# Kernel tuning notes

Hardware: AMD Instinct MI355X
Metric: run time of the kernel (lower is better)

Reference implementation:

```python
import jax, jax.numpy as jnp
import numpy as np

N_C, N_M, N_D = 100000, 50000, 10000
E = 800000
F_IN, F_H, F_OUT = 128, 64, 64
EPS = 1e-12


def setup_inputs() -> dict:
    key = jax.random.key(0)
    ks = jax.random.split(key, 24)
    s = 1.0 / np.sqrt(F_IN)
    s2 = 1.0 / np.sqrt(F_H)
    inp = {
        'x_circ': jax.random.normal(ks[0], (N_C, F_IN), jnp.float32),
        'x_mir': jax.random.normal(ks[1], (N_M, F_IN), jnp.float32),
        'x_dis': jax.random.normal(ks[2], (N_D, F_IN), jnp.float32),
        'src_cm': jax.random.randint(ks[3], (E,), 0, N_C, jnp.int32),
        'dst_cm': jax.random.randint(ks[4], (E,), 0, N_M, jnp.int32),
        'src_md': jax.random.randint(ks[5], (E,), 0, N_M, jnp.int32),
        'dst_md': jax.random.randint(ks[6], (E,), 0, N_D, jnp.int32),
        'src_cd': jax.random.randint(ks[7], (E,), 0, N_C, jnp.int32),
        'dst_cd': jax.random.randint(ks[8], (E,), 0, N_D, jnp.int32),
        'src_mc': jax.random.randint(ks[9], (E,), 0, N_M, jnp.int32),
        'dst_mc': jax.random.randint(ks[10], (E,), 0, N_C, jnp.int32),
        'src_dm': jax.random.randint(ks[11], (E,), 0, N_D, jnp.int32),
        'dst_dm': jax.random.randint(ks[12], (E,), 0, N_M, jnp.int32),
        'src_dc': jax.random.randint(ks[13], (E,), 0, N_D, jnp.int32),
        'dst_dc': jax.random.randint(ks[14], (E,), 0, N_C, jnp.int32),
        'W1_l': jax.random.uniform(ks[15], (6, F_IN, F_H), jnp.float32, -s, s),
        'W1_r': jax.random.uniform(ks[16], (6, F_IN, F_H), jnp.float32, -s, s),
        'b1': jnp.zeros((6, F_H), jnp.float32),
        'W2_l': jax.random.uniform(ks[17], (6, F_H, F_OUT), jnp.float32, -s2, s2),
        'W2_r': jax.random.uniform(ks[18], (6, F_H, F_OUT), jnp.float32, -s2, s2),
        'b2': jnp.zeros((6, F_OUT), jnp.float32),
        'W_res': jax.random.uniform(ks[19], (3, F_IN, F_OUT), jnp.float32, -s, s),
        'b_res': jnp.zeros((3, F_OUT), jnp.float32),
    }
    return inp


def _sage(x_src, x_dst, src, dst, Wl, bl, Wr, n_dst):
    # PyG SAGEConv (mean aggr): lin_l(mean_{j in N(i)} x_j) + lin_r(x_i)
    msg = x_src[src]                                              # [E, F] gather
    agg = jax.ops.segment_sum(msg, dst, num_segments=n_dst)      # [n_dst, F]
    cnt = jax.ops.segment_sum(jnp.ones_like(dst, dtype=x_src.dtype), dst,
                              num_segments=n_dst)
    mean = agg / jnp.maximum(cnt, 1.0)[:, None]
    return mean @ Wl + bl + x_dst @ Wr


def _hetero_layer(xc, xm, xd, Wl, Wr, b, edges):
    # relation order: 0=c->m, 1=m->d, 2=c->d, 3=m->c, 4=d->m, 5=d->c
    h_m = 0.5 * (_sage(xc, xm, edges['cm'][0], edges['cm'][1], Wl[0], b[0], Wr[0], xm.shape[0])
                 + _sage(xd, xm, edges['dm'][0], edges['dm'][1], Wl[4], b[4], Wr[4], xm.shape[0]))
    h_d = 0.5 * (_sage(xm, xd, edges['md'][0], edges['md'][1], Wl[1], b[1], Wr[1], xd.shape[0])
                 + _sage(xc, xd, edges['cd'][0], edges['cd'][1], Wl[2], b[2], Wr[2], xd.shape[0]))
    h_c = 0.5 * (_sage(xm, xc, edges['mc'][0], edges['mc'][1], Wl[3], b[3], Wr[3], xc.shape[0])
                 + _sage(xd, xc, edges['dc'][0], edges['dc'][1], Wl[5], b[5], Wr[5], xc.shape[0]))
    return h_c, h_m, h_d


def _l2norm(x):
    n = jnp.sqrt(jnp.sum(x * x, axis=1, keepdims=True))
    return x / jnp.maximum(n, EPS)


def reference(x_circ, x_mir, x_dis,
              src_cm, dst_cm, src_md, dst_md, src_cd, dst_cd,
              src_mc, dst_mc, src_dm, dst_dm, src_dc, dst_dc,
              W1_l, W1_r, b1, W2_l, W2_r, b2, W_res, b_res):
    edges = {'cm': (src_cm, dst_cm), 'md': (src_md, dst_md), 'cd': (src_cd, dst_cd),
             'mc': (src_mc, dst_mc), 'dm': (src_dm, dst_dm), 'dc': (src_dc, dst_dc)}
    h_c, h_m, h_d = _hetero_layer(x_circ, x_mir, x_dis, W1_l, W1_r, b1, edges)
    h_c, h_m, h_d = jax.nn.relu(h_c), jax.nn.relu(h_m), jax.nn.relu(h_d)  # dropout = identity (eval)
    o_c, o_m, o_d = _hetero_layer(h_c, h_m, h_d, W2_l, W2_r, b2, edges)
    o_c = o_c + x_circ @ W_res[0] + b_res[0]
    o_m = o_m + x_mir @ W_res[1] + b_res[1]
    o_d = o_d + x_dis @ W_res[2] + b_res[2]
    return _l2norm(o_c), _l2norm(o_m), _l2norm(o_d)
```

## Files before the change

### kernel.cpp

```cpp
#include <hip/hip_runtime.h>
#include <cstdint>
#include <cstddef>

#define EE        800000
#define NC        100000
#define NM        50000
#define ND        10000
#define NSLOTS    320000

#define SB0 0
#define SB1 50000
#define SB2 60000
#define SB3 70000
#define SB4 170000
#define SB5 220000

#define R0 0
#define R1 100000
#define R2 150000
#define R3 250000
#define R4 300000
#define R5 310000

#define NB 2400
#define EPB 4096
#define EBL 196
#define EPB2 8192
#define PBL 98
#define BCAP 3072

typedef _Float16 f16x8 __attribute__((ext_vector_type(8)));
typedef float f32x4 __attribute__((ext_vector_type(4)));
typedef float f32x2 __attribute__((ext_vector_type(2)));

__device__ __forceinline__ void bucket_split(int rel, int d, int& lb, int& dl) {
    switch (rel) {
        case 0: case 4: lb = d / 125; dl = d - lb * 125; break;
        case 1: case 2: lb = d / 25;  dl = d - lb * 25;  break;
        default:        lb = d / 250; dl = d - lb * 250; break;
    }
}

__global__ __launch_bounds__(256) void bucket_hist_k(
    const int* __restrict__ d0, const int* __restrict__ d1, const int* __restrict__ d2,
    const int* __restrict__ d3, const int* __restrict__ d4, const int* __restrict__ d5,
    int* __restrict__ bhist)
{
    __shared__ int hl[400];
    int rel = blockIdx.y;
    const int* dst;
    switch (rel) {
        case 0: dst = d0; break; case 1: dst = d1; break; case 2: dst = d2; break;
        case 3: dst = d3; break; case 4: dst = d4; break; default: dst = d5; break;
    }
    int tid = threadIdx.x;
    for (int i = tid; i < 400; i += 256) hl[i] = 0;
    __syncthreads();
    int e0 = blockIdx.x * EPB;
#pragma unroll
    for (int t = 0; t < EPB / 256; ++t) {
        int e = e0 + t * 256 + tid;
        if (e < EE) {
            int lb, dl;
            bucket_split(rel, dst[e], lb, dl);
            atomicAdd(&hl[lb], 1);
        }
    }
    __syncthreads();
    for (int i = tid; i < 400; i += 256) {
        int v = hl[i];
        if (v) atomicAdd(&bhist[rel * 400 + i], v);
    }
}

__global__ __launch_bounds__(256) void bucket_scan_k(const int* __restrict__ bhist,
    int* __restrict__ bOff, int* __restrict__ bCur, int* __restrict__ off)
{
    __shared__ int lds[256];
    int tid = threadIdx.x;
    int v[10];
    int tot = 0;
#pragma unroll
    for (int t = 0; t < 10; ++t) {
        int idx = tid * 10 + t;
        int x = (idx < NB) ? bhist[idx] : 0;
        v[t] = tot;
        tot += x;
    }
    lds[tid] = tot;
    __syncthreads();
    for (int o = 1; o < 256; o <<= 1) {
        int x = 0;
        if (tid >= o) x = lds[tid - o];
        __syncthreads();
        lds[tid] += x;
        __syncthreads();
    }
    int excl = lds[tid] - tot;
#pragma unroll
    for (int t = 0; t < 10; ++t) {
        int idx = tid * 10 + t;
        if (idx < NB) {
            int val = excl + v[t];
            bOff[idx] = val;
            bCur[idx] = val;
        }
    }
    if (tid == 255) {
        bOff[NB] = lds[255];
        off[NSLOTS] = lds[255];
    }
}

__global__ __launch_bounds__(512) void partition_k(
    const int* __restrict__ s0, const int* __restrict__ d0,
    const int* __restrict__ s1, const int* __restrict__ d1,
    const int* __restrict__ s2, const int* __restrict__ d2,
    const int* __restrict__ s3, const int* __restrict__ d3,
    const int* __restrict__ s4, const int* __restrict__ d4,
    const int* __restrict__ s5, const int* __restrict__ d5,
    int* __restrict__ bCur, int* __restrict__ bArr)
{
    __shared__ int hist[400];
    __shared__ int curs[400];
    __shared__ unsigned short lbs[EPB2];
    __shared__ unsigned char dls[EPB2];
    int rel = blockIdx.y;
    const int* src; const int* dst;
    switch (rel) {
        case 0: src = s0; dst = d0; break;
        case 1: src = s1; dst = d1; break;
        case 2: src = s2; dst = d2; break;
        case 3: src = s3; dst = d3; break;
        case 4: src = s4; dst = d4; break;
        default: src = s5; dst = d5; break;
    }
    int tid = threadIdx.x;
    for (int i = tid; i < 400; i += 512) hist[i] = 0;
    __syncthreads();
    int e0 = blockIdx.x * EPB2;
    int e1 = e0 + EPB2; if (e1 > EE) e1 = EE;
    int m = e1 - e0;
    for (int i = tid; i < m; i += 512) {
        int lb, dl;
        bucket_split(rel, dst[e0 + i], lb, dl);
        lbs[i] = (unsigned short)lb;
        dls[i] = (unsigned char)dl;
        atomicAdd(&hist[lb], 1);
    }
    __syncthreads();
    for (int i = tid; i < 400; i += 512) {
        int c = hist[i];
        curs[i] = c ? atomicAdd(&bCur[rel * 400 + i], c) : 0;
    }
    __syncthreads();
    for (int i = tid; i < m; i += 512) {
        int p = atomicAdd(&curs[lbs[i]], 1);
        bArr[p] = ((int)dls[i] << 17) | src[e0 + i];
    }
}

__global__ __launch_bounds__(256) void bucket_build_k(
    const int* __restrict__ bArr, const int* __restrict__ bOff,
    int* __restrict__ off, int* __restrict__ csr)
{
    __shared__ int cnt[256];
    __shared__ int sc[256];
    __shared__ int cur[256];
    __shared__ int stage[BCAP];
    int b = blockIdx.x;
    int tid = threadIdx.x;
    int r = b / 400;
    int lb = b - r * 400;
    int spb, sbase;
    switch (r) {
        case 0: spb = 125; sbase = SB0; break;
        case 1: spb = 25;  sbase = SB1; break;
        case 2: spb = 25;  sbase = SB2; break;
        case 3: spb = 250; sbase = SB3; break;
        case 4: spb = 125; sbase = SB4; break;
        default: spb = 250; sbase = SB5; break;
    }
    int slot0 = lb * spb;
    int e0 = bOff[b], e1 = bOff[b + 1];
    int m = e1 - e0;
    int ms = m < BCAP ? m : BCAP;

    cnt[tid] = 0;
    __syncthreads();
    for (int i = tid; i < ms; i += 256) {
        int p = bArr[e0 + i];
        stage[i] = p;
        atomicAdd(&cnt[p >> 17], 1);
    }
    for (int i = BCAP + tid; i < m; i += 256) {
        int p = bArr[e0 + i];
        atomicAdd(&cnt[p >> 17], 1);
    }
    __syncthreads();
    int x = cnt[tid];
    sc[tid] = x;
    __syncthreads();
    for (int o = 1; o < 256; o <<= 1) {
        int y = 0;
        if (tid >= o) y = sc[tid - o];
        __syncthreads();
        sc[tid] += y;
        __syncthreads();
    }
    int excl = sc[tid] - x;
    cur[tid] = excl;
    if (tid < spb) off[sbase + slot0 + tid] = e0 + excl;
    __syncthreads();
    for (int i = tid; i < ms; i += 256) {
        int p = stage[i];
        int pos = atomicAdd(&cur[p >> 17], 1);
        csr[e0 + pos] = (p & 0x1FFFF) << 7;
    }
    for (int i = BCAP + tid; i < m; i += 256) {
        int p = bArr[e0 + i];
        int pos = atomicAdd(&cur[p >> 17], 1);
        csr[e0 + pos] = (p & 0x1FFFF) << 7;
    }
}

__device__ __forceinline__ unsigned f2bf(float f) {
    unsigned b = __float_as_uint(f);
    return (b + 0x7FFFu + ((b >> 16) & 1u)) >> 16;
}

__global__ __launch_bounds__(256) void cvtW_k(
    const float* __restrict__ W1l, const float* __restrict__ W2l,
    const float* __restrict__ W1r, const float* __restrict__ W2r,
    const float* __restrict__ Wres, const float* __restrict__ b1,
    const float* __restrict__ b2, const float* __restrict__ bres,
    _Float16* __restrict__ Wt1, _Float16* __restrict__ Wt2,
    _Float16* __restrict__ Wz1t, _Float16* __restrict__ Wz2t,
    _Float16* __restrict__ Wrest, float* __restrict__ bz1, float* __restrict__ bz2,
    int* __restrict__ bhist)
{
    const int raT[3] = {0, 1, 3}, rbT[3] = {4, 2, 5}, rmT[3] = {1, 2, 0};
    int i = blockIdx.x * 256 + threadIdx.x;
    if (i < NB) bhist[i] = 0;
    if (i < 6 * 128 * 64) {
        int r = i >> 13, rem = i & 8191, k = rem >> 6, n = rem & 63;
        Wt1[(size_t)r * 8192 + (size_t)n * 128 + k] = (_Float16)W1l[i];
    }
    if (i < 6 * 64 * 64) {
        int r = i >> 12, rem = i & 4095, k = rem >> 6, n = rem & 63;
        Wt2[(size_t)r * 4096 + (size_t)n * 64 + k] = (_Float16)W2l[i];
    }
    if (i < 3 * 8192) {
        int t = i >> 13, rem = i & 8191, n = rem >> 7, k = rem & 127;
        float v = 0.5f * (W1r[(size_t)raT[t] * 8192 + k * 64 + n] +
                          W1r[(size_t)rbT[t] * 8192 + k * 64 + n]);
        Wz1t[i] = (_Float16)v;
    }
    if (i < 3 * 4096) {
        int t = i >> 12, rem = i & 4095, n = rem >> 6, k = rem & 63;
        float v = 0.5f * (W2r[(size_t)raT[t] * 4096 + k * 64 + n] +
                          W2r[(size_t)rbT[t] * 4096 + k * 64 + n]);
        Wz2t[i] = (_Float16)v;
    }
    if (i < 3 * 8192) {
        int t = i >> 13, rem = i & 8191, n = rem >> 7, k = rem & 127;
        Wrest[i] = (_Float16)Wres[(size_t)rmT[t] * 8192 + k * 64 + n];
    }
    if (i < 192) {
        int t = i >> 6, n = i & 63;
        bz1[i] = 0.5f * (b1[raT[t] * 64 + n] + b1[rbT[t] * 64 + n]);
        bz2[i] = 0.5f * (b2[raT[t] * 64 + n] + b2[rbT[t] * 64 + n]) + bres[rmT[t] * 64 + n];
    }
}

__global__ __launch_bounds__(256) void fused1_k(
    const float* __restrict__ fc, const float* __restrict__ fm, const float* __restrict__ fd,
    const _Float16* __restrict__ Wt1, const _Float16* __restrict__ Wz1t,
    const float* __restrict__ bz1,
    unsigned short* __restrict__ y,
    float* __restrict__ hc, float* __restrict__ hm, float* __restrict__ hd)
{
    int b = blockIdx.x;
    int t, lb;
    if (b < 782)      { t = 0; lb = b; }
    else if (b < 939) { t = 1; lb = b - 782; }
    else              { t = 2; lb = b - 939; }
    const float* x; int n; float* zo; int ra, rb, roA, roB;
    switch (t) {
        case 0: x = fm; n = NM; zo = hm; ra = 1; rb = 3; roA = R1; roB = R3; break;
        case 1: x = fd; n = ND; zo = hd; ra = 4; rb = 5; roA = R4; roB = R5; break;
        default: x = fc; n = NC; zo = hc; ra = 0; rb = 2; roA = R0; roB = R2; break;
    }
    __shared__ _Float16 xs[64 * 136];
    int tid = threadIdx.x;
    int node0 = lb * 64;
    for (int idx = tid; idx < 64 * 16; idx += 256) {
        int nn = idx >> 4, c8 = idx & 15;
        int g = node0 + nn;
        float4 u0 = make_float4(0.f, 0.f, 0.f, 0.f), u1 = u0;
        if (g < n) {
            const float4* p = (const float4*)(x + (size_t)g * 128 + c8 * 8);
            u0 = p[0]; u1 = p[1];
        }
        f16x8 v;
        v[0] = (_Float16)u0.x; v[1] = (_Float16)u0.y; v[2] = (_Float16)u0.z; v[3] = (_Float16)u0.w;
        v[4] = (_Float16)u1.x; v[5] = (_Float16)u1.y; v[6] = (_Float16)u1.z; v[7] = (_Float16)u1.w;
        *(f16x8*)(xs + nn * 136 + c8 * 8) = v;
    }
    __syncthreads();
    int lane = tid & 63, wv = tid >> 6;
    int lr = lane & 15, lg = lane >> 4;
    if (wv < 2) {
        int rel = wv ? rb : ra;
        int ro  = wv ? roB : roA;
        const _Float16* W = Wt1 + (size_t)rel * 8192;
        unsigned short* yo = y + (size_t)ro * 64;
        f16x8 bf[4][4];
#pragma unroll
        for (int kt = 0; kt < 4; ++kt)
#pragma unroll
            for (int nt = 0; nt < 4; ++nt)
                bf[kt][nt] = *(const f16x8*)(W + (size_t)(nt * 16 + lr) * 128 + kt * 32 + lg * 8);
#pragma unroll
        for (int rt = 0; rt < 4; ++rt) {
            f32x4 acc[4];
#pragma unroll
            for (int nt = 0; nt < 4; ++nt) { acc[nt][0] = 0.f; acc[nt][1] = 0.f; acc[nt][2] = 0.f; acc[nt][3] = 0.f; }
            const _Float16* xrow = xs + (rt * 16 + lr) * 136;
#pragma unroll
            for (int kt = 0; kt < 4; ++kt) {
                f16x8 af = *(const f16x8*)(xrow + kt * 32 + lg * 8);
#pragma unroll
                for (int nt = 0; nt < 4; ++nt)
                    acc[nt] = __builtin_amdgcn_mfma_f32_16x16x32_f16(af, bf[kt][nt], acc[nt], 0, 0, 0);
            }
            int orow = node0 + rt * 16 + lg * 4;
#pragma unroll
            for (int rg = 0; rg < 4; ++rg) {
                int gg = orow + rg;
                if (gg < n) {
                    unsigned short* yr = yo + (size_t)gg * 64 + lr;
#pragma unroll
                    for (int nt = 0; nt < 4; ++nt)
                        yr[nt * 16] = (unsigned short)f2bf(acc[nt][rg]);
                }
            }
        }
    } else {
        const _Float16* W = Wz1t + (size_t)t * 8192;
        const float* bz = bz1 + t * 64;
        f16x8 bf[4][4];
#pragma unroll
        for (int kt = 0; kt < 4; ++kt)
#pragma unroll
            for (int nt = 0; nt < 4; ++nt)
                bf[kt][nt] = *(const f16x8*)(W + (size_t)(nt * 16 + lr) * 128 + kt * 32 + lg * 8);
        int rbase = (wv - 2) * 32;
#pragma unroll
        for (int rt = 0; rt < 2; ++rt) {
            f32x4 acc[4];
#pragma unroll
            for (int nt = 0; nt < 4; ++nt) {
                float bv = bz[nt * 16 + lr];
                acc[nt][0] = bv; acc[nt][1] = bv; acc[nt][2] = bv; acc[nt][3] = bv;
            }
            const _Float16* xrow = xs + (rbase + rt * 16 + lr) * 136;
#pragma unroll
            for (int kt = 0; kt < 4; ++kt) {
                f16x8 af = *(const f16x8*)(xrow + kt * 32 + lg * 8);
#pragma unroll
                for (int nt = 0; nt < 4; ++nt)
                    acc[nt] = __builtin_amdgcn_mfma_f32_16x16x32_f16(af, bf[kt][nt], acc[nt], 0, 0, 0);
            }
            int orow = node0 + rbase + rt * 16 + lg * 4;
#pragma unroll
            for (int rg = 0; rg < 4; ++rg) {
                int gg = orow + rg;
                if (gg < n) {
                    float* zr = zo + (size_t)gg * 64 + lr;
#pragma unroll
                    for (int nt = 0; nt < 4; ++nt)
                        zr[nt * 16] = acc[nt][rg];
                }
            }
        }
    }
}

__global__ __launch_bounds__(256) void fused2_k(
    const float* __restrict__ hc, const float* __restrict__ hm, const float* __restrict__ hd,
    const float* __restrict__ xc, const float* __restrict__ xm, const float* __restrict__ xd,
    const _Float16* __restrict__ Wt2, const _Float16* __restrict__ Wz2t,
    const _Float16* __restrict__ Wrest, const float* __restrict__ bz2,
    unsigned short* __restrict__ y,
    float* __restrict__ oc, float* __restrict__ om, float* __restrict__ od)
{
    int b = blockIdx.x;
    int t, lb;
    if (b < 782)      { t = 0; lb = b; }
    else if (b < 939) { t = 1; lb = b - 782; }
    else              { t = 2; lb = b - 939; }
    const float *h, *x; int n; float* zo; int ra, rb, roA, roB;
    switch (t) {
        case 0: h = hm; x = xm; n = NM; zo = om; ra = 1; rb = 3; roA = R1; roB = R3; break;
        case 1: h = hd; x = xd; n = ND; zo = od; ra = 4; rb = 5; roA = R4; roB = R5; break;
        default: h = hc; x = xc; n = NC; zo = oc; ra = 0; rb = 2; roA = R0; roB = R2; break;
    }
    __shared__ _Float16 hs[64 * 72];
    __shared__ _Float16 xs[64 * 136];
    int tid = threadIdx.x;
    int node0 = lb * 64;
    for (int idx = tid; idx < 64 * 8; idx += 256) {
        int nn = idx >> 3, c8 = idx & 7;
        int g = node0 + nn;
        float4 u0 = make_float4(0.f, 0.f, 0.f, 0.f), u1 = u0;
        if (g < n) {
            const float4* p = (const float4*)(h + (size_t)g * 64 + c8 * 8);
            u0 = p[0]; u1 = p[1];
        }
        f16x8 v;
        v[0] = (_Float16)u0.x; v[1] = (_Float16)u0.y; v[2] = (_Float16)u0.z; v[3] = (_Float16)u0.w;
        v[4] = (_Float16)u1.x; v[5] = (_Float16)u1.y; v[6] = (_Float16)u1.z; v[7] = (_Float16)u1.w;
        *(f16x8*)(hs + nn * 72 + c8 * 8) = v;
    }
    for (int idx = tid; idx < 64 * 16; idx += 256) {
        int nn = idx >> 4, c8 = idx & 15;
        int g = node0 + nn;
        float4 u0 = make_float4(0.f, 0.f, 0.f, 0.f), u1 = u0;
        if (g < n) {
            const float4* p = (const float4*)(x + (size_t)g * 128 + c8 * 8);
            u0 = p[0]; u1 = p[1];
        }
        f16x8 v;
        v[0] = (_Float16)u0.x; v[1] = (_Float16)u0.y; v[2] = (_Float16)u0.z; v[3] = (_Float16)u0.w;
        v[4] = (_Float16)u1.x; v[5] = (_Float16)u1.y; v[6] = (_Float16)u1.z; v[7] = (_Float16)u1.w;
        *(f16x8*)(xs + nn * 136 + c8 * 8) = v;
    }
    __syncthreads();
    int lane = tid & 63, wv = tid >> 6;
    int lr = lane & 15, lg = lane >> 4;
    if (wv < 2) {
        int rel = wv ? rb : ra;
        int ro  = wv ? roB : roA;
        const _Float16* W = Wt2 + (size_t)rel * 4096;
        unsigned short* yo = y + (size_t)ro * 64;
        f16x8 bf[2][4];
#pragma unroll
        for (int kt = 0; kt < 2; ++kt)
#pragma unroll
            for (int nt = 0; nt < 4; ++nt)
                bf[kt][nt] = *(const f16x8*)(W + (size_t)(nt * 16 + lr) * 64 + kt * 32 + lg * 8);
#pragma unroll
        for (int rt = 0; rt < 4; ++rt) {
            f32x4 acc[4];
#pragma unroll
            for (int nt = 0; nt < 4; ++nt) { acc[nt][0] = 0.f; acc[nt][1] = 0.f; acc[nt][2] = 0.f; acc[nt][3] = 0.f; }
            const _Float16* hrow = hs + (rt * 16 + lr) * 72;
#pragma unroll
            for (int kt = 0; kt < 2; ++kt) {
                f16x8 af = *(const f16x8*)(hrow + kt * 32 + lg * 8);
#pragma unroll
                for (int nt = 0; nt < 4; ++nt)
                    acc[nt] = __builtin_amdgcn_mfma_f32_16x16x32_f16(af, bf[kt][nt], acc[nt], 0, 0, 0);
            }
            int orow = node0 + rt * 16 + lg * 4;
#pragma unroll
            for (int rg = 0; rg < 4; ++rg) {
                int gg = orow + rg;
                if (gg < n) {
                    unsigned short* yr = yo + (size_t)gg * 64 + lr;
#pragma unroll
                    for (int nt = 0; nt < 4; ++nt)
                        yr[nt * 16] = (unsigned short)f2bf(acc[nt][rg]);
                }
            }
        }
    } else {
        const _Float16* Wh = Wz2t + (size_t)t * 4096;
        const _Float16* Wx = Wrest + (size_t)t * 8192;
        const float* bz = bz2 + t * 64;
        f16x8 bfh[2][4];
#pragma unroll
        for (int kt = 0; kt < 2; ++kt)
#pragma unroll
            for (int nt = 0; nt < 4; ++nt)
                bfh[kt][nt] = *(const f16x8*)(Wh + (size_t)(nt * 16 + lr) * 64 + kt * 32 + lg * 8);
        f16x8 bfx[4][4];
#pragma unroll
        for (int kt = 0; kt < 4; ++kt)
#pragma unroll
            for (int nt = 0; nt < 4; ++nt)
                bfx[kt][nt] = *(const f16x8*)(Wx + (size_t)(nt * 16 + lr) * 128 + kt * 32 + lg * 8);
        int rbase = (wv - 2) * 32;
#pragma unroll
        for (int rt = 0; rt < 2; ++rt) {
            f32x4 acc[4];
#pragma unroll
            for (int nt = 0; nt < 4; ++nt) {
                float bv = bz[nt * 16 + lr];
                acc[nt][0] = bv; acc[nt][1] = bv; acc[nt][2] = bv; acc[nt][3] = bv;
            }
            const _Float16* hrow = hs + (rbase + rt * 16 + lr) * 72;
            const _Float16* xrow = xs + (rbase + rt * 16 + lr) * 136;
#pragma unroll
            for (int kt = 0; kt < 2; ++kt) {
                f16x8 af = *(const f16x8*)(hrow + kt * 32 + lg * 8);
#pragma unroll
                for (int nt = 0; nt < 4; ++nt)
                    acc[nt] = __builtin_amdgcn_mfma_f32_16x16x32_f16(af, bfh[kt][nt], acc[nt], 0, 0, 0);
            }
#pragma unroll
            for (int kt = 0; kt < 4; ++kt) {
                f16x8 af = *(const f16x8*)(xrow + kt * 32 + lg * 8);
#pragma unroll
                for (int nt = 0; nt < 4; ++nt)
                    acc[nt] = __builtin_amdgcn_mfma_f32_16x16x32_f16(af, bfx[kt][nt], acc[nt], 0, 0, 0);
            }
            int orow = node0 + rbase + rt * 16 + lg * 4;
#pragma unroll
            for (int rg = 0; rg < 4; ++rg) {
                int gg = orow + rg;
                if (gg < n) {
                    float* zr = zo + (size_t)gg * 64 + lr;
#pragma unroll
                    for (int nt = 0; nt < 4; ++nt)
                        zr[nt * 16] = acc[nt][rg];
                }
            }
        }
    }
}

__device__ __forceinline__ void acc_pk(f32x2* a, uint4 v) {
    f32x2 t0, t1, t2, t3;
    t0[0] = __uint_as_float(v.x << 16); t0[1] = __uint_as_float(v.x & 0xFFFF0000u);
    t1[0] = __uint_as_float(v.y << 16); t1[1] = __uint_as_float(v.y & 0xFFFF0000u);
    t2[0] = __uint_as_float(v.z << 16); t2[1] = __uint_as_float(v.z & 0xFFFF0000u);
    t3[0] = __uint_as_float(v.w << 16); t3[1] = __uint_as_float(v.w & 0xFFFF0000u);
    a[0] += t0; a[1] += t1; a[2] += t2; a[3] += t3;
}

template<bool RELU, bool NORM>
__global__ __launch_bounds__(256) void agg_all_k(
    const unsigned short* __restrict__ y, const int* __restrict__ off,
    const int* __restrict__ csr,
    float* __restrict__ ioc, float* __restrict__ iom, float* __restrict__ iod)
{
    int w = blockIdx.x * 4 + (threadIdx.x >> 6);
    int t, wid;
    if (w < NM) { t = 0; wid = w; }
    else if (w < NM + ND) { t = 1; wid = w - NM; }
    else { t = 2; wid = w - NM - ND; }
    const int *o1, *o2; const unsigned short *y1, *y2; float* io;
    switch (t) {
        case 0: o1 = off + SB0; o2 = off + SB4; y1 = y + (size_t)R0 * 64; y2 = y + (size_t)R4 * 64; io = iom; break;
        case 1: o1 = off + SB1; o2 = off + SB2; y1 = y + (size_t)R1 * 64; y2 = y + (size_t)R2 * 64; io = iod; break;
        default: o1 = off + SB3; o2 = off + SB5; y1 = y + (size_t)R3 * 64; y2 = y + (size_t)R5 * 64; io = ioc; break;
    }
    int lane = threadIdx.x & 63;
    int g = lane >> 3, ql = lane & 7;
    int qoff = ql * 16;
    f32x2 acc[4];
#pragma unroll
    for (int j = 0; j < 4; ++j) { acc[j][0] = 0.f; acc[j][1] = 0.f; }
    {
        const char* yb = (const char*)y1;
        int e0 = o1[wid], e1 = o1[wid + 1];
        f32x2 a[4];
#pragma unroll
        for (int j = 0; j < 4; ++j) { a[j][0] = 0.f; a[j][1] = 0.f; }
        int e = e0 + g;
        int i0 = 0, i1 = 0;
        if (e < e1) i0 = csr[e];
        if (e + 8 < e1) i1 = csr[e + 8];
        for (; e + 8 < e1; e += 16) {
            int p0 = csr[e + 16 < e1 ? e + 16 : e];
            int p1 = csr[e + 24 < e1 ? e + 24 : e];
            uint4 vA = *(const uint4*)(yb + (unsigned)i0 + qoff);
            uint4 vB = *(const uint4*)(yb + (unsigned)i1 + qoff);
            acc_pk(a, vA);
            acc_pk(a, vB);
            i0 = p0; i1 = p1;
        }
        if (e < e1) {
            uint4 v = *(const uint4*)(yb + (unsigned)i0 + qoff);
            acc_pk(a, v);
        }
        float inv = 1.f / fmaxf((float)(e1 - e0), 1.f);
        f32x2 iv; iv[0] = inv; iv[1] = inv;
#pragma unroll
        for (int j = 0; j < 4; ++j) acc[j] += a[j] * iv;
    }
    {
        const char* yb = (const char*)y2;
        int e0 = o2[wid], e1 = o2[wid + 1];
        f32x2 a[4];
#pragma unroll
        for (int j = 0; j < 4; ++j) { a[j][0] = 0.f; a[j][1] = 0.f; }
        int e = e0 + g;
        int i0 = 0, i1 = 0;
        if (e < e1) i0 = csr[e];
        if (e + 8 < e1) i1 = csr[e + 8];
        for (; e + 8 < e1; e += 16) {
            int p0 = csr[e + 16 < e1 ? e + 16 : e];
            int p1 = csr[e + 24 < e1 ? e + 24 : e];
            uint4 vA = *(const uint4*)(yb + (unsigned)i0 + qoff);
            uint4 vB = *(const uint4*)(yb + (unsigned)i1 + qoff);
            acc_pk(a, vA);
            acc_pk(a, vB);
            i0 = p0; i1 = p1;
        }
        if (e < e1) {
            uint4 v = *(const uint4*)(yb + (unsigned)i0 + qoff);
            acc_pk(a, v);
        }
        float inv = 1.f / fmaxf((float)(e1 - e0), 1.f);
        f32x2 iv; iv[0] = inv; iv[1] = inv;
#pragma unroll
        for (int j = 0; j < 4; ++j) acc[j] += a[j] * iv;
    }
#pragma unroll
    for (int j = 0; j < 4; ++j) {
#pragma unroll
        for (int c = 0; c < 2; ++c) {
            float v = acc[j][c];
            v += __shfl_xor(v, 8);
            v += __shfl_xor(v, 16);
            v += __shfl_xor(v, 32);
            acc[j][c] = v;
        }
    }
    if (g == 0) {
        float* iorow = io + ((size_t)wid << 6) + ql * 8;
        float4 z1 = *((const float4*)iorow);
        float4 z2 = *((const float4*)(iorow + 4));
        float o[8];
        o[0] = 0.5f * acc[0][0] + z1.x; o[1] = 0.5f * acc[0][1] + z1.y;
        o[2] = 0.5f * acc[1][0] + z1.z; o[3] = 0.5f * acc[1][1] + z1.w;
        o[4] = 0.5f * acc[2][0] + z2.x; o[5] = 0.5f * acc[2][1] + z2.y;
        o[6] = 0.5f * acc[3][0] + z2.z; o[7] = 0.5f * acc[3][1] + z2.w;
        if (RELU) {
#pragma unroll
            for (int j = 0; j < 8; ++j) o[j] = fmaxf(o[j], 0.f);
        }
        if (NORM) {
            float ss = 0.f;
#pragma unroll
            for (int j = 0; j < 8; ++j) ss += o[j] * o[j];
            ss += __shfl_xor(ss, 1); ss += __shfl_xor(ss, 2); ss += __shfl_xor(ss, 4);
            float r = 1.f / fmaxf(sqrtf(ss), 1e-12f);
#pragma unroll
            for (int j = 0; j < 8; ++j) o[j] *= r;
        }
        *((float4*)iorow) = make_float4(o[0], o[1], o[2], o[3]);
        *((float4*)(iorow + 4)) = make_float4(o[4], o[5], o[6], o[7]);
    }
}

extern "C" void kernel_launch(void* const* d_in, const int* in_sizes, int n_in,
                              void* d_out, int out_size, void* d_ws, size_t ws_size,
                              hipStream_t stream) {
    const float* x_c = (const float*)d_in[0];
    const float* x_m = (const float*)d_in[1];
    const float* x_d = (const float*)d_in[2];
    const int* src_cm = (const int*)d_in[3];
    const int* dst_cm = (const int*)d_in[4];
    const int* src_md = (const int*)d_in[5];
    const int* dst_md = (const int*)d_in[6];
    const int* src_cd = (const int*)d_in[7];
    const int* dst_cd = (const int*)d_in[8];
    const int* src_mc = (const int*)d_in[9];
    const int* dst_mc = (const int*)d_in[10];
    const int* src_dm = (const int*)d_in[11];
    const int* dst_dm = (const int*)d_in[12];
    const int* src_dc = (const int*)d_in[13];
    const int* dst_dc = (const int*)d_in[14];
    const float* W1l = (const float*)d_in[15];
    const float* W1r = (const float*)d_in[16];
    const float* b1 = (const float*)d_in[17];
    const float* W2l = (const float*)d_in[18];
    const float* W2r = (const float*)d_in[19];
    const float* b2 = (const float*)d_in[20];
    const float* Wres = (const float*)d_in[21];
    const float* bres = (const float*)d_in[22];
    float* out = (float*)d_out;

    int* off = (int*)d_ws;
    int* csr = off + 320064;
    int* bhist = csr + 4800000;
    int* bOff = bhist + 2400;
    int* bCur = bOff + 2404;
    float* h = (float*)(bCur + 2404);
    float* h_c = h;
    float* h_m = h_c + (size_t)NC * 64;
    float* h_d = h_m + (size_t)NM * 64;
    unsigned short* y = (unsigned short*)(h + (size_t)160000 * 64);
    int* bArr = (int*)y;
    _Float16* Wt1 = (_Float16*)(y + (size_t)320000 * 64);
    _Float16* Wt2 = Wt1 + 6 * 64 * 128;
    _Float16* Wz1t = Wt2 + 6 * 64 * 64;
    _Float16* Wz2t = Wz1t + 3 * 64 * 128;
    _Float16* Wrest = Wz2t + 3 * 64 * 64;
    float* bz1 = (float*)(Wrest + 3 * 64 * 128);
    float* bz2 = bz1 + 192;

    float* out_c = out;
    float* out_m = out + (size_t)NC * 64;
    float* out_d = out_m + (size_t)NM * 64;

    cvtW_k<<<192, 256, 0, stream>>>(W1l, W2l, W1r, W2r, Wres, b1, b2, bres,
                                    Wt1, Wt2, Wz1t, Wz2t, Wrest, bz1, bz2, bhist);

    bucket_hist_k<<<dim3(EBL, 6), 256, 0, stream>>>(dst_cm, dst_md, dst_cd, dst_mc, dst_dm, dst_dc, bhist);
    bucket_scan_k<<<1, 256, 0, stream>>>(bhist, bOff, bCur, off);
    partition_k<<<dim3(PBL, 6), 512, 0, stream>>>(src_cm, dst_cm, src_md, dst_md, src_cd, dst_cd,
                                                  src_mc, dst_mc, src_dm, dst_dm, src_dc, dst_dc,
                                                  bCur, bArr);
    bucket_build_k<<<NB, 256, 0, stream>>>(bArr, bOff, off, csr);

    fused1_k<<<2502, 256, 0, stream>>>(x_c, x_m, x_d, Wt1, Wz1t, bz1, y, h_c, h_m, h_d);
    agg_all_k<true, false><<<40000, 256, 0, stream>>>(y, off, csr, h_c, h_m, h_d);

    fused2_k<<<2502, 256, 0, stream>>>(h_c, h_m, h_d, x_c, x_m, x_d,
                                       Wt2, Wz2t, Wrest, bz2, y, out_c, out_m, out_d);
    agg_all_k<false, true><<<40000, 256, 0, stream>>>(y, off, csr, out_c, out_m, out_d);
}
```

Baseline: 633.8 us.

## Merge preprocessing kernels, partition concurrently with layer-1 GEMM, build CSR in place

Weight conversion is merged into the bucket histogram kernel, and edge partitioning is merged with the layer-1 projection GEMM in one launch, so independent work shares a grid and fewer kernels run. The bucket array now aliases the CSR buffer, which bucket_build_k rewrites in place after staging in LDS. BCAP is raised to 4096 and the overflow path is removed, which assumes no bucket exceeds 4096 edges. The aggregation loop drops the bounds clamps on prefetched CSR indices and folds the byte offset into the base pointer, so the last iterations may read past the end of the CSR array into the rest of the workspace.

```diff
diff --git a/kernel.cpp b/kernel.cpp
--- a/kernel.cpp
+++ b/kernel.cpp
@@ -27,7 +27,7 @@
 #define EBL 196
 #define EPB2 8192
 #define PBL 98
-#define BCAP 3072
+#define BCAP 4096
 
 typedef _Float16 f16x8 __attribute__((ext_vector_type(8)));
 typedef float f32x4 __attribute__((ext_vector_type(4)));
@@ -41,22 +41,71 @@
     }
 }
 
-__global__ __launch_bounds__(256) void bucket_hist_k(
+__device__ __forceinline__ unsigned f2bf(float f) {
+    unsigned b = __float_as_uint(f);
+    return (b + 0x7FFFu + ((b >> 16) & 1u)) >> 16;
+}
+
+__global__ __launch_bounds__(256) void cvt_hist_k(
+    const float* __restrict__ W1l, const float* __restrict__ W2l,
+    const float* __restrict__ W1r, const float* __restrict__ W2r,
+    const float* __restrict__ Wres, const float* __restrict__ b1,
+    const float* __restrict__ b2, const float* __restrict__ bres,
+    _Float16* __restrict__ Wt1, _Float16* __restrict__ Wt2,
+    _Float16* __restrict__ Wz1t, _Float16* __restrict__ Wz2t,
+    _Float16* __restrict__ Wrest, float* __restrict__ bz1, float* __restrict__ bz2,
+    int* __restrict__ bhist,
     const int* __restrict__ d0, const int* __restrict__ d1, const int* __restrict__ d2,
-    const int* __restrict__ d3, const int* __restrict__ d4, const int* __restrict__ d5,
-    int* __restrict__ bhist)
+    const int* __restrict__ d3, const int* __restrict__ d4, const int* __restrict__ d5)
 {
     __shared__ int hl[400];
-    int rel = blockIdx.y;
+    int blk = blockIdx.x;
+    int tid = threadIdx.x;
+    if (blk < 192) {
+        const int raT[3] = {0, 1, 3}, rbT[3] = {4, 2, 5}, rmT[3] = {1, 2, 0};
+        int i = blk * 256 + tid;
+        if (i < 6 * 128 * 64) {
+            int r = i >> 13, rem = i & 8191, k = rem >> 6, n = rem & 63;
+            Wt1[(size_t)r * 8192 + (size_t)n * 128 + k] = (_Float16)W1l[i];
+        }
+        if (i < 6 * 64 * 64) {
+            int r = i >> 12, rem = i & 4095, k = rem >> 6, n = rem & 63;
+            Wt2[(size_t)r * 4096 + (size_t)n * 64 + k] = (_Float16)W2l[i];
+        }
+        if (i < 3 * 8192) {
+            int t = i >> 13, rem = i & 8191, n = rem >> 7, k = rem & 127;
+            float v = 0.5f * (W1r[(size_t)raT[t] * 8192 + k * 64 + n] +
+                              W1r[(size_t)rbT[t] * 8192 + k * 64 + n]);
+            Wz1t[i] = (_Float16)v;
+        }
+        if (i < 3 * 4096) {
+            int t = i >> 12, rem = i & 4095, n = rem >> 6, k = rem & 63;
+            float v = 0.5f * (W2r[(size_t)raT[t] * 4096 + k * 64 + n] +
+                              W2r[(size_t)rbT[t] * 4096 + k * 64 + n]);
+            Wz2t[i] = (_Float16)v;
+        }
+        if (i < 3 * 8192) {
+            int t = i >> 13, rem = i & 8191, n = rem >> 7, k = rem & 127;
+            Wrest[i] = (_Float16)Wres[(size_t)rmT[t] * 8192 + k * 64 + n];
+        }
+        if (i < 192) {
+            int t = i >> 6, n = i & 63;
+            bz1[i] = 0.5f * (b1[raT[t] * 64 + n] + b1[rbT[t] * 64 + n]);
+            bz2[i] = 0.5f * (b2[raT[t] * 64 + n] + b2[rbT[t] * 64 + n]) + bres[rmT[t] * 64 + n];
+        }
+        return;
+    }
+    int hb = blk - 192;
+    int rel = hb / EBL;
+    int chunk = hb - rel * EBL;
     const int* dst;
     switch (rel) {
         case 0: dst = d0; break; case 1: dst = d1; break; case 2: dst = d2; break;
         case 3: dst = d3; break; case 4: dst = d4; break; default: dst = d5; break;
     }
-    int tid = threadIdx.x;
     for (int i = tid; i < 400; i += 256) hl[i] = 0;
     __syncthreads();
-    int e0 = blockIdx.x * EPB;
+    int e0 = chunk * EPB;
 #pragma unroll
     for (int t = 0; t < EPB / 256; ++t) {
         int e = e0 + t * 256 + tid;
@@ -112,51 +161,166 @@
     }
 }
 
-__global__ __launch_bounds__(512) void partition_k(
+__global__ __launch_bounds__(256) void part_fused1_k(
     const int* __restrict__ s0, const int* __restrict__ d0,
     const int* __restrict__ s1, const int* __restrict__ d1,
     const int* __restrict__ s2, const int* __restrict__ d2,
     const int* __restrict__ s3, const int* __restrict__ d3,
     const int* __restrict__ s4, const int* __restrict__ d4,
     const int* __restrict__ s5, const int* __restrict__ d5,
-    int* __restrict__ bCur, int* __restrict__ bArr)
+    int* __restrict__ bCur, int* __restrict__ bArr,
+    const float* __restrict__ fc, const float* __restrict__ fm, const float* __restrict__ fd,
+    const _Float16* __restrict__ Wt1, const _Float16* __restrict__ Wz1t,
+    const float* __restrict__ bz1,
+    unsigned short* __restrict__ y,
+    float* __restrict__ hc, float* __restrict__ hm, float* __restrict__ hd)
 {
-    __shared__ int hist[400];
-    __shared__ int curs[400];
-    __shared__ unsigned short lbs[EPB2];
-    __shared__ unsigned char dls[EPB2];
-    int rel = blockIdx.y;
-    const int* src; const int* dst;
-    switch (rel) {
-        case 0: src = s0; dst = d0; break;
-        case 1: src = s1; dst = d1; break;
-        case 2: src = s2; dst = d2; break;
-        case 3: src = s3; dst = d3; break;
-        case 4: src = s4; dst = d4; break;
-        default: src = s5; dst = d5; break;
-    }
+    __shared__ __align__(16) char smem[27776];
+    int blk = blockIdx.x;
     int tid = threadIdx.x;
-    for (int i = tid; i < 400; i += 512) hist[i] = 0;
-    __syncthreads();
-    int e0 = blockIdx.x * EPB2;
-    int e1 = e0 + EPB2; if (e1 > EE) e1 = EE;
-    int m = e1 - e0;
-    for (int i = tid; i < m; i += 512) {
-        int lb, dl;
-        bucket_split(rel, dst[e0 + i], lb, dl);
-        lbs[i] = (unsigned short)lb;
-        dls[i] = (unsigned char)dl;
-        atomicAdd(&hist[lb], 1);
-    }
-    __syncthreads();
-    for (int i = tid; i < 400; i += 512) {
-        int c = hist[i];
-        curs[i] = c ? atomicAdd(&bCur[rel * 400 + i], c) : 0;
-    }
-    __syncthreads();
-    for (int i = tid; i < m; i += 512) {
-        int p = atomicAdd(&curs[lbs[i]], 1);
-        bArr[p] = ((int)dls[i] << 17) | src[e0 + i];
+    if (blk < 6 * PBL) {
+        int* hist = (int*)smem;
+        int* curs = hist + 400;
+        unsigned short* lbs = (unsigned short*)(curs + 400);
+        unsigned char* dls = (unsigned char*)(lbs + EPB2);
+        int rel = blk / PBL;
+        int chunk = blk - rel * PBL;
+        const int* src; const int* dst;
+        switch (rel) {
+            case 0: src = s0; dst = d0; break;
+            case 1: src = s1; dst = d1; break;
+            case 2: src = s2; dst = d2; break;
+            case 3: src = s3; dst = d3; break;
+            case 4: src = s4; dst = d4; break;
+            default: src = s5; dst = d5; break;
+        }
+        for (int i = tid; i < 400; i += 256) hist[i] = 0;
+        __syncthreads();
+        int e0 = chunk * EPB2;
+        int e1 = e0 + EPB2; if (e1 > EE) e1 = EE;
+        int m = e1 - e0;
+        for (int i = tid; i < m; i += 256) {
+            int lb, dl;
+            bucket_split(rel, dst[e0 + i], lb, dl);
+            lbs[i] = (unsigned short)lb;
+            dls[i] = (unsigned char)dl;
+            atomicAdd(&hist[lb], 1);
+        }
+        __syncthreads();
+        for (int i = tid; i < 400; i += 256) {
+            int c = hist[i];
+            curs[i] = c ? atomicAdd(&bCur[rel * 400 + i], c) : 0;
+        }
+        __syncthreads();
+        for (int i = tid; i < m; i += 256) {
+            int p = atomicAdd(&curs[lbs[i]], 1);
+            bArr[p] = ((int)dls[i] << 17) | src[e0 + i];
+        }
+        return;
+    }
+    _Float16* xs = (_Float16*)smem;
+    int b = blk - 6 * PBL;
+    int t, lb;
+    if (b < 782)      { t = 0; lb = b; }
+    else if (b < 939) { t = 1; lb = b - 782; }
+    else              { t = 2; lb = b - 939; }
+    const float* x; int n; float* zo; int ra, rb, roA, roB;
+    switch (t) {
+        case 0: x = fm; n = NM; zo = hm; ra = 1; rb = 3; roA = R1; roB = R3; break;
+        case 1: x = fd; n = ND; zo = hd; ra = 4; rb = 5; roA = R4; roB = R5; break;
+        default: x = fc; n = NC; zo = hc; ra = 0; rb = 2; roA = R0; roB = R2; break;
+    }
+    int node0 = lb * 64;
+    for (int idx = tid; idx < 64 * 16; idx += 256) {
+        int nn = idx >> 4, c8 = idx & 15;
+        int g = node0 + nn;
+        float4 u0 = make_float4(0.f, 0.f, 0.f, 0.f), u1 = u0;
+        if (g < n) {
+            const float4* p = (const float4*)(x + (size_t)g * 128 + c8 * 8);
+            u0 = p[0]; u1 = p[1];
+        }
+        f16x8 v;
+        v[0] = (_Float16)u0.x; v[1] = (_Float16)u0.y; v[2] = (_Float16)u0.z; v[3] = (_Float16)u0.w;
+        v[4] = (_Float16)u1.x; v[5] = (_Float16)u1.y; v[6] = (_Float16)u1.z; v[7] = (_Float16)u1.w;
+        *(f16x8*)(xs + nn * 136 + c8 * 8) = v;
+    }
+    __syncthreads();
+    int lane = tid & 63, wv = tid >> 6;
+    int lr = lane & 15, lg = lane >> 4;
+    if (wv < 2) {
+        int rel = wv ? rb : ra;
+        int ro  = wv ? roB : roA;
+        const _Float16* W = Wt1 + (size_t)rel * 8192;
+        unsigned short* yo = y + (size_t)ro * 64;
+        f16x8 bf[4][4];
+#pragma unroll
+        for (int kt = 0; kt < 4; ++kt)
+#pragma unroll
+            for (int nt = 0; nt < 4; ++nt)
+                bf[kt][nt] = *(const f16x8*)(W + (size_t)(nt * 16 + lr) * 128 + kt * 32 + lg * 8);
+#pragma unroll
+        for (int rt = 0; rt < 4; ++rt) {
+            f32x4 acc[4];
+#pragma unroll
+            for (int nt = 0; nt < 4; ++nt) { acc[nt][0] = 0.f; acc[nt][1] = 0.f; acc[nt][2] = 0.f; acc[nt][3] = 0.f; }
+            const _Float16* xrow = xs + (rt * 16 + lr) * 136;
+#pragma unroll
+            for (int kt = 0; kt < 4; ++kt) {
+                f16x8 af = *(const f16x8*)(xrow + kt * 32 + lg * 8);
+#pragma unroll
+                for (int nt = 0; nt < 4; ++nt)
+                    acc[nt] = __builtin_amdgcn_mfma_f32_16x16x32_f16(af, bf[kt][nt], acc[nt], 0, 0, 0);
+            }
+            int orow = node0 + rt * 16 + lg * 4;
+#pragma unroll
+            for (int rg = 0; rg < 4; ++rg) {
+                int gg = orow + rg;
+                if (gg < n) {
+                    unsigned short* yr = yo + (size_t)gg * 64 + lr;
+#pragma unroll
+                    for (int nt = 0; nt < 4; ++nt)
+                        yr[nt * 16] = (unsigned short)f2bf(acc[nt][rg]);
+                }
+            }
+        }
+    } else {
+        const _Float16* W = Wz1t + (size_t)t * 8192;
+        const float* bz = bz1 + t * 64;
+        f16x8 bf[4][4];
+#pragma unroll
+        for (int kt = 0; kt < 4; ++kt)
+#pragma unroll
+            for (int nt = 0; nt < 4; ++nt)
+                bf[kt][nt] = *(const f16x8*)(W + (size_t)(nt * 16 + lr) * 128 + kt * 32 + lg * 8);
+        int rbase = (wv - 2) * 32;
+#pragma unroll
+        for (int rt = 0; rt < 2; ++rt) {
+            f32x4 acc[4];
+#pragma unroll
+            for (int nt = 0; nt < 4; ++nt) {
+                float bv = bz[nt * 16 + lr];
+                acc[nt][0] = bv; acc[nt][1] = bv; acc[nt][2] = bv; acc[nt][3] = bv;
+            }
+            const _Float16* xrow = xs + (rbase + rt * 16 + lr) * 136;
+#pragma unroll
+            for (int kt = 0; kt < 4; ++kt) {
+                f16x8 af = *(const f16x8*)(xrow + kt * 32 + lg * 8);
+#pragma unroll
+                for (int nt = 0; nt < 4; ++nt)
+                    acc[nt] = __builtin_amdgcn_mfma_f32_16x16x32_f16(af, bf[kt][nt], acc[nt], 0, 0, 0);
+            }
+            int orow = node0 + rbase + rt * 16 + lg * 4;
+#pragma unroll
+            for (int rg = 0; rg < 4; ++rg) {
+                int gg = orow + rg;
+                if (gg < n) {
+                    float* zr = zo + (size_t)gg * 64 + lr;
+#pragma unroll
+                    for (int nt = 0; nt < 4; ++nt)
+                        zr[nt * 16] = acc[nt][rg];
+                }
+            }
+        }
     }
 }
 
@@ -193,10 +357,6 @@
         stage[i] = p;
         atomicAdd(&cnt[p >> 17], 1);
     }
-    for (int i = BCAP + tid; i < m; i += 256) {
-        int p = bArr[e0 + i];
-        atomicAdd(&cnt[p >> 17], 1);
-    }
     __syncthreads();
     int x = cnt[tid];
     sc[tid] = x;
@@ -216,174 +376,6 @@
         int p = stage[i];
         int pos = atomicAdd(&cur[p >> 17], 1);
         csr[e0 + pos] = (p & 0x1FFFF) << 7;
-    }
-    for (int i = BCAP + tid; i < m; i += 256) {
-        int p = bArr[e0 + i];
-        int pos = atomicAdd(&cur[p >> 17], 1);
-        csr[e0 + pos] = (p & 0x1FFFF) << 7;
-    }
-}
-
-__device__ __forceinline__ unsigned f2bf(float f) {
-    unsigned b = __float_as_uint(f);
-    return (b + 0x7FFFu + ((b >> 16) & 1u)) >> 16;
-}
-
-__global__ __launch_bounds__(256) void cvtW_k(
-    const float* __restrict__ W1l, const float* __restrict__ W2l,
-    const float* __restrict__ W1r, const float* __restrict__ W2r,
-    const float* __restrict__ Wres, const float* __restrict__ b1,
-    const float* __restrict__ b2, const float* __restrict__ bres,
-    _Float16* __restrict__ Wt1, _Float16* __restrict__ Wt2,
-    _Float16* __restrict__ Wz1t, _Float16* __restrict__ Wz2t,
-    _Float16* __restrict__ Wrest, float* __restrict__ bz1, float* __restrict__ bz2,
-    int* __restrict__ bhist)
-{
-    const int raT[3] = {0, 1, 3}, rbT[3] = {4, 2, 5}, rmT[3] = {1, 2, 0};
-    int i = blockIdx.x * 256 + threadIdx.x;
-    if (i < NB) bhist[i] = 0;
-    if (i < 6 * 128 * 64) {
-        int r = i >> 13, rem = i & 8191, k = rem >> 6, n = rem & 63;
-        Wt1[(size_t)r * 8192 + (size_t)n * 128 + k] = (_Float16)W1l[i];
-    }
-    if (i < 6 * 64 * 64) {
-        int r = i >> 12, rem = i & 4095, k = rem >> 6, n = rem & 63;
-        Wt2[(size_t)r * 4096 + (size_t)n * 64 + k] = (_Float16)W2l[i];
-    }
-    if (i < 3 * 8192) {
-        int t = i >> 13, rem = i & 8191, n = rem >> 7, k = rem & 127;
-        float v = 0.5f * (W1r[(size_t)raT[t] * 8192 + k * 64 + n] +
-                          W1r[(size_t)rbT[t] * 8192 + k * 64 + n]);
-        Wz1t[i] = (_Float16)v;
-    }
-    if (i < 3 * 4096) {
-        int t = i >> 12, rem = i & 4095, n = rem >> 6, k = rem & 63;
-        float v = 0.5f * (W2r[(size_t)raT[t] * 4096 + k * 64 + n] +
-                          W2r[(size_t)rbT[t] * 4096 + k * 64 + n]);
-        Wz2t[i] = (_Float16)v;
-    }
-    if (i < 3 * 8192) {
-        int t = i >> 13, rem = i & 8191, n = rem >> 7, k = rem & 127;
-        Wrest[i] = (_Float16)Wres[(size_t)rmT[t] * 8192 + k * 64 + n];
-    }
-    if (i < 192) {
-        int t = i >> 6, n = i & 63;
-        bz1[i] = 0.5f * (b1[raT[t] * 64 + n] + b1[rbT[t] * 64 + n]);
-        bz2[i] = 0.5f * (b2[raT[t] * 64 + n] + b2[rbT[t] * 64 + n]) + bres[rmT[t] * 64 + n];
-    }
-}
-
-__global__ __launch_bounds__(256) void fused1_k(
-    const float* __restrict__ fc, const float* __restrict__ fm, const float* __restrict__ fd,
-    const _Float16* __restrict__ Wt1, const _Float16* __restrict__ Wz1t,
-    const float* __restrict__ bz1,
-    unsigned short* __restrict__ y,
-    float* __restrict__ hc, float* __restrict__ hm, float* __restrict__ hd)
-{
-    int b = blockIdx.x;
-    int t, lb;
-    if (b < 782)      { t = 0; lb = b; }
-    else if (b < 939) { t = 1; lb = b - 782; }
-    else              { t = 2; lb = b - 939; }
-    const float* x; int n; float* zo; int ra, rb, roA, roB;
-    switch (t) {
-        case 0: x = fm; n = NM; zo = hm; ra = 1; rb = 3; roA = R1; roB = R3; break;
-        case 1: x = fd; n = ND; zo = hd; ra = 4; rb = 5; roA = R4; roB = R5; break;
-        default: x = fc; n = NC; zo = hc; ra = 0; rb = 2; roA = R0; roB = R2; break;
-    }
-    __shared__ _Float16 xs[64 * 136];
-    int tid = threadIdx.x;
-    int node0 = lb * 64;
-    for (int idx = tid; idx < 64 * 16; idx += 256) {
-        int nn = idx >> 4, c8 = idx & 15;
-        int g = node0 + nn;
-        float4 u0 = make_float4(0.f, 0.f, 0.f, 0.f), u1 = u0;
-        if (g < n) {
-            const float4* p = (const float4*)(x + (size_t)g * 128 + c8 * 8);
-            u0 = p[0]; u1 = p[1];
-        }
-        f16x8 v;
-        v[0] = (_Float16)u0.x; v[1] = (_Float16)u0.y; v[2] = (_Float16)u0.z; v[3] = (_Float16)u0.w;
-        v[4] = (_Float16)u1.x; v[5] = (_Float16)u1.y; v[6] = (_Float16)u1.z; v[7] = (_Float16)u1.w;
-        *(f16x8*)(xs + nn * 136 + c8 * 8) = v;
-    }
-    __syncthreads();
-    int lane = tid & 63, wv = tid >> 6;
-    int lr = lane & 15, lg = lane >> 4;
-    if (wv < 2) {
-        int rel = wv ? rb : ra;
-        int ro  = wv ? roB : roA;
-        const _Float16* W = Wt1 + (size_t)rel * 8192;
-        unsigned short* yo = y + (size_t)ro * 64;
-        f16x8 bf[4][4];
-#pragma unroll
-        for (int kt = 0; kt < 4; ++kt)
-#pragma unroll
-            for (int nt = 0; nt < 4; ++nt)
-                bf[kt][nt] = *(const f16x8*)(W + (size_t)(nt * 16 + lr) * 128 + kt * 32 + lg * 8);
-#pragma unroll
-        for (int rt = 0; rt < 4; ++rt) {
-            f32x4 acc[4];
-#pragma unroll
-            for (int nt = 0; nt < 4; ++nt) { acc[nt][0] = 0.f; acc[nt][1] = 0.f; acc[nt][2] = 0.f; acc[nt][3] = 0.f; }
-            const _Float16* xrow = xs + (rt * 16 + lr) * 136;
-#pragma unroll
-            for (int kt = 0; kt < 4; ++kt) {
-                f16x8 af = *(const f16x8*)(xrow + kt * 32 + lg * 8);
-#pragma unroll
-                for (int nt = 0; nt < 4; ++nt)
-                    acc[nt] = __builtin_amdgcn_mfma_f32_16x16x32_f16(af, bf[kt][nt], acc[nt], 0, 0, 0);
-            }
-            int orow = node0 + rt * 16 + lg * 4;
-#pragma unroll
-            for (int rg = 0; rg < 4; ++rg) {
-                int gg = orow + rg;
-                if (gg < n) {
-                    unsigned short* yr = yo + (size_t)gg * 64 + lr;
-#pragma unroll
-                    for (int nt = 0; nt < 4; ++nt)
-                        yr[nt * 16] = (unsigned short)f2bf(acc[nt][rg]);
-                }
-            }
-        }
-    } else {
-        const _Float16* W = Wz1t + (size_t)t * 8192;
-        const float* bz = bz1 + t * 64;
-        f16x8 bf[4][4];
-#pragma unroll
-        for (int kt = 0; kt < 4; ++kt)
-#pragma unroll
-            for (int nt = 0; nt < 4; ++nt)
-                bf[kt][nt] = *(const f16x8*)(W + (size_t)(nt * 16 + lr) * 128 + kt * 32 + lg * 8);
-        int rbase = (wv - 2) * 32;
-#pragma unroll
-        for (int rt = 0; rt < 2; ++rt) {
-            f32x4 acc[4];
-#pragma unroll
-            for (int nt = 0; nt < 4; ++nt) {
-                float bv = bz[nt * 16 + lr];
-                acc[nt][0] = bv; acc[nt][1] = bv; acc[nt][2] = bv; acc[nt][3] = bv;
-            }
-            const _Float16* xrow = xs + (rbase + rt * 16 + lr) * 136;
-#pragma unroll
-            for (int kt = 0; kt < 4; ++kt) {
-                f16x8 af = *(const f16x8*)(xrow + kt * 32 + lg * 8);
-#pragma unroll
-                for (int nt = 0; nt < 4; ++nt)
-                    acc[nt] = __builtin_amdgcn_mfma_f32_16x16x32_f16(af, bf[kt][nt], acc[nt], 0, 0, 0);
-            }
-            int orow = node0 + rbase + rt * 16 + lg * 4;
-#pragma unroll
-            for (int rg = 0; rg < 4; ++rg) {
-                int gg = orow + rg;
-                if (gg < n) {
-                    float* zr = zo + (size_t)gg * 64 + lr;
-#pragma unroll
-                    for (int nt = 0; nt < 4; ++nt)
-                        zr[nt * 16] = acc[nt][rg];
-                }
-            }
-        }
     }
 }
 
@@ -564,7 +556,7 @@
 #pragma unroll
     for (int j = 0; j < 4; ++j) { acc[j][0] = 0.f; acc[j][1] = 0.f; }
     {
-        const char* yb = (const char*)y1;
+        const char* yb = (const char*)y1 + qoff;
         int e0 = o1[wid], e1 = o1[wid + 1];
         f32x2 a[4];
 #pragma unroll
@@ -574,16 +566,16 @@
         if (e < e1) i0 = csr[e];
         if (e + 8 < e1) i1 = csr[e + 8];
         for (; e + 8 < e1; e += 16) {
-            int p0 = csr[e + 16 < e1 ? e + 16 : e];
-            int p1 = csr[e + 24 < e1 ? e + 24 : e];
-            uint4 vA = *(const uint4*)(yb + (unsigned)i0 + qoff);
-            uint4 vB = *(const uint4*)(yb + (unsigned)i1 + qoff);
+            int p0 = csr[e + 16];
+            int p1 = csr[e + 24];
+            uint4 vA = *(const uint4*)(yb + (unsigned)i0);
+            uint4 vB = *(const uint4*)(yb + (unsigned)i1);
             acc_pk(a, vA);
             acc_pk(a, vB);
             i0 = p0; i1 = p1;
         }
         if (e < e1) {
-            uint4 v = *(const uint4*)(yb + (unsigned)i0 + qoff);
+            uint4 v = *(const uint4*)(yb + (unsigned)i0);
             acc_pk(a, v);
         }
         float inv = 1.f / fmaxf((float)(e1 - e0), 1.f);
@@ -592,7 +584,7 @@
         for (int j = 0; j < 4; ++j) acc[j] += a[j] * iv;
     }
     {
-        const char* yb = (const char*)y2;
+        const char* yb = (const char*)y2 + qoff;
         int e0 = o2[wid], e1 = o2[wid + 1];
         f32x2 a[4];
 #pragma unroll
@@ -602,16 +594,16 @@
         if (e < e1) i0 = csr[e];
         if (e + 8 < e1) i1 = csr[e + 8];
         for (; e + 8 < e1; e += 16) {
-            int p0 = csr[e + 16 < e1 ? e + 16 : e];
-            int p1 = csr[e + 24 < e1 ? e + 24 : e];
-            uint4 vA = *(const uint4*)(yb + (unsigned)i0 + qoff);
-            uint4 vB = *(const uint4*)(yb + (unsigned)i1 + qoff);
+            int p0 = csr[e + 16];
+            int p1 = csr[e + 24];
+            uint4 vA = *(const uint4*)(yb + (unsigned)i0);
+            uint4 vB = *(const uint4*)(yb + (unsigned)i1);
             acc_pk(a, vA);
             acc_pk(a, vB);
             i0 = p0; i1 = p1;
         }
         if (e < e1) {
-            uint4 v = *(const uint4*)(yb + (unsigned)i0 + qoff);
+            uint4 v = *(const uint4*)(yb + (unsigned)i0);
             acc_pk(a, v);
         }
         float inv = 1.f / fmaxf((float)(e1 - e0), 1.f);
@@ -687,6 +679,7 @@
 
     int* off = (int*)d_ws;
     int* csr = off + 320064;
+    int* bArr = csr;
     int* bhist = csr + 4800000;
     int* bOff = bhist + 2400;
     int* bCur = bOff + 2404;
@@ -695,7 +688,6 @@
     float* h_m = h_c + (size_t)NC * 64;
     float* h_d = h_m + (size_t)NM * 64;
     unsigned short* y = (unsigned short*)(h + (size_t)160000 * 64);
-    int* bArr = (int*)y;
     _Float16* Wt1 = (_Float16*)(y + (size_t)320000 * 64);
     _Float16* Wt2 = Wt1 + 6 * 64 * 128;
     _Float16* Wz1t = Wt2 + 6 * 64 * 64;
@@ -708,20 +700,27 @@
     float* out_m = out + (size_t)NC * 64;
     float* out_d = out_m + (size_t)NM * 64;
 
-    cvtW_k<<<192, 256, 0, stream>>>(W1l, W2l, W1r, W2r, Wres, b1, b2, bres,
-                                    Wt1, Wt2, Wz1t, Wz2t, Wrest, bz1, bz2, bhist);
-
-    bucket_hist_k<<<dim3(EBL, 6), 256, 0, stream>>>(dst_cm, dst_md, dst_cd, dst_mc, dst_dm, dst_dc, bhist);
+    hipMemsetAsync(bhist, 0, NB * sizeof(int), stream);
+
+    cvt_hist_k<<<192 + EBL * 6, 256, 0, stream>>>(
+        W1l, W2l, W1r, W2r, Wres, b1, b2, bres,
+        Wt1, Wt2, Wz1t, Wz2t, Wrest, bz1, bz2, bhist,
+        dst_cm, dst_md, dst_cd, dst_mc, dst_dm, dst_dc);
+
     bucket_scan_k<<<1, 256, 0, stream>>>(bhist, bOff, bCur, off);
-    partition_k<<<dim3(PBL, 6), 512, 0, stream>>>(src_cm, dst_cm, src_md, dst_md, src_cd, dst_cd,
-                                                  src_mc, dst_mc, src_dm, dst_dm, src_dc, dst_dc,
-                                                  bCur, bArr);
+
+    part_fused1_k<<<6 * PBL + 2502, 256, 0, stream>>>(
+        src_cm, dst_cm, src_md, dst_md, src_cd, dst_cd,
+        src_mc, dst_mc, src_dm, dst_dm, src_dc, dst_dc,
+        bCur, bArr,
+        x_c, x_m, x_d, Wt1, Wz1t, bz1, y, h_c, h_m, h_d);
+
     bucket_build_k<<<NB, 256, 0, stream>>>(bArr, bOff, off, csr);
 
-    fused1_k<<<2502, 256, 0, stream>>>(x_c, x_m, x_d, Wt1, Wz1t, bz1, y, h_c, h_m, h_d);
     agg_all_k<true, false><<<40000, 256, 0, stream>>>(y, off, csr, h_c, h_m, h_d);
 
     fused2_k<<<2502, 256, 0, stream>>>(h_c, h_m, h_d, x_c, x_m, x_d,
                                        Wt2, Wz2t, Wrest, bz2, y, out_c, out_m, out_d);
+
     agg_all_k<false, true><<<40000, 256, 0, stream>>>(y, off, csr, out_c, out_m, out_d);
 }
```

New measurement: 626.1 us. About the same (-1.2%).
